# Performance work log

Measured on AMD Instinct MI355X. Metric: run time of the kernel, lower is better.

Reference implementation:

```python
import jax, jax.numpy as jnp
import numpy as np

B, N, HW, PS, FHW = 16, 4096, 224, 8, 56

def _gelu(x):
    return jax.nn.gelu(x, approximate=True)  # tanh approximation, matches nn.GELU(approximate='tanh')

def _conv(x, w, b, stride):
    y = jax.lax.conv_general_dilated(x, w, (stride, stride), [(1, 1), (1, 1)],
                                     dimension_numbers=('NCHW', 'OIHW', 'NCHW'))
    return y + b[None, :, None, None]

def _embed(points):
    # for i in 0..11: append sin(2^i * p) then cos(2^i * p) -> [B,N,48]
    factors = 2.0 ** jnp.arange(12, dtype=points.dtype)
    scaled = points[..., None, :] * factors[:, None]          # [B,N,12,2]
    feats = jnp.concatenate([jnp.sin(scaled), jnp.cos(scaled)], axis=-1)  # [B,N,12,4]
    return feats.reshape(points.shape[0], points.shape[1], 48)

def _extract_patches(fmap, points):
    # fmap [B,C,H,W]; points in [0,1]; bilinear grid_sample, zeros padding, align_corners=True
    Bq, C, H, W = fmap.shape
    centers = points * 2.0 - 1.0
    step = 2.0 / (W - 1)
    half = (PS - 1) / 2.0
    offs = jnp.linspace(-half, half, PS, dtype=fmap.dtype) * step
    offx2d, offy2d = jnp.meshgrid(offs, offs, indexing='ij')   # [ps,ps]
    gx = centers[..., 0][..., None, None] + offx2d             # [B,N,ps,ps]
    gy = centers[..., 1][..., None, None] + offy2d
    # align_corners=True pixel coords
    ix = (gx + 1.0) * 0.5 * (W - 1)
    iy = (gy + 1.0) * 0.5 * (H - 1)
    x0f = jnp.floor(ix); y0f = jnp.floor(iy)
    x0 = x0f.astype(jnp.int32); y0 = y0f.astype(jnp.int32)
    x1 = x0 + 1; y1 = y0 + 1
    wx1 = ix - x0f; wx0 = 1.0 - wx1
    wy1 = iy - y0f; wy0 = 1.0 - wy1
    fflat = fmap.reshape(Bq, C, H * W)

    def corner(xi, yi, w):
        valid = ((xi >= 0) & (xi < W) & (yi >= 0) & (yi < H)).astype(fmap.dtype)
        idx = jnp.clip(yi, 0, H - 1) * W + jnp.clip(xi, 0, W - 1)   # [B,N,ps,ps]
        vals = jax.vmap(lambda f, i: f[:, i])(fflat, idx)           # [B,C,N,ps,ps]
        return vals * (w * valid)[:, None]

    out = (corner(x0, y0, wx0 * wy0) + corner(x1, y0, wx1 * wy0)
           + corner(x0, y1, wx0 * wy1) + corner(x1, y1, wx1 * wy1))  # [B,C,N,ps,ps]
    return out.transpose(0, 2, 1, 3, 4)                              # [B,N,C,ps,ps]

def setup_inputs():
    key = jax.random.key(0)
    ks = jax.random.split(key, 26)
    def w(k, shape):
        fan_in = int(np.prod(shape[1:]))
        return jax.random.normal(k, shape, jnp.float32) * (1.0 / np.sqrt(fan_in))
    inp = {
        'points': jax.random.uniform(ks[0], (B, N, 2), jnp.float32),
        'images': jax.random.normal(ks[1], (B, 3, HW, HW), jnp.float32),
        # plane encoder
        'pw1': w(ks[2], (16, 3, 3, 3)),  'pb1': jnp.zeros((16,), jnp.float32),
        'pw2': w(ks[3], (32, 16, 3, 3)), 'pb2': jnp.zeros((32,), jnp.float32),
        'pw3': w(ks[4], (4, 32, 3, 3)),  'pb3': jnp.zeros((4,), jnp.float32),
        # global encoder
        'gw1': w(ks[5], (4, 3, 3, 3)),   'gb1': jnp.zeros((4,), jnp.float32),
        'gw2': w(ks[6], (8, 4, 3, 3)),   'gb2': jnp.zeros((8,), jnp.float32),
        'gw3': w(ks[7], (16, 8, 3, 3)),  'gb3': jnp.zeros((16,), jnp.float32),
        'gw4': w(ks[8], (32, 16, 3, 3)), 'gb4': jnp.zeros((32,), jnp.float32),
        'gw5': w(ks[9], (64, 32, 3, 3)), 'gb5': jnp.zeros((64,), jnp.float32),
        # point encoder (torch Linear: [out,in])
        'lw1': w(ks[10], (256, 48)),  'lb1': jnp.zeros((256,), jnp.float32),
        'lw2': w(ks[11], (256, 256)), 'lb2': jnp.zeros((256,), jnp.float32),
        # head
        'hw1': w(ks[12], (512, 576)), 'hb1': jnp.zeros((512,), jnp.float32),
        'hw2': w(ks[13], (1, 512)),   'hb2': jnp.zeros((1,), jnp.float32),
    }
    return inp

def reference(points, images, pw1, pb1, pw2, pb2, pw3, pb3,
              gw1, gb1, gw2, gb2, gw3, gb3, gw4, gb4, gw5, gb5,
              lw1, lb1, lw2, lb2, hw1, hb1, hw2, hb2):
    # point branch
    pe = _embed(points)                                         # [B,N,48]
    pf = _gelu(pe @ lw1.T + lb1) @ lw2.T + lb2                  # [B,N,256]
    # plane encoder -> 4x56x56 fmap
    f = _gelu(_conv(images, pw1, pb1, 2))
    f = _gelu(_conv(f, pw2, pb2, 2))
    fmap = _gelu(_conv(f, pw3, pb3, 1))                         # [B,4,56,56]
    # global encoder -> [B,64]
    g = images
    for wg, bg in ((gw1, gb1), (gw2, gb2), (gw3, gb3), (gw4, gb4), (gw5, gb5)):
        g = _gelu(_conv(g, wg, bg, 2))
    gc = g.mean(axis=(2, 3))                                    # AvgPool2d(7)+Flatten -> [B,64]
    gc = jnp.broadcast_to(gc[:, None, :], (points.shape[0], points.shape[1], 64))
    # per-point bilinear patch gather
    patches = _extract_patches(fmap, points).reshape(points.shape[0], points.shape[1], -1)  # [B,N,256]
    fused = jnp.concatenate([pf, patches, gc], axis=-1)         # [B,N,576]
    logit = _gelu(fused @ hw1.T + hb1) @ hw2.T + hb2            # [B,N,1]
    return logit
```

## Files before the change

kernel.cpp:

```cpp
#include <hip/hip_runtime.h>
#include <math.h>

#define BB 16
#define NN 4096
#define M_TOT (BB*NN)
#define HBK 64

typedef __attribute__((ext_vector_type(8))) short s8v;
typedef __attribute__((ext_vector_type(4))) float f4v;

__device__ __forceinline__ float gelu_t(float x){
    float u = 1.5957691216057308f * x * (1.0f + 0.044715f*x*x);
    return x / (1.0f + __expf(-u));
}

__device__ __forceinline__ unsigned short f2bf(float f){
    unsigned int u = __float_as_uint(f);
    u += 0x7fffu + ((u >> 16) & 1u);
    return (unsigned short)(u >> 16);
}

#define GLL(src, dst) __builtin_amdgcn_global_load_lds( \
    (const __attribute__((address_space(1))) void*)(src), \
    (__attribute__((address_space(3))) void*)(dst), 16, 0, 0)

template<int CIN, int COUT, int STRIDE, int CHUNK>
__device__ __forceinline__ void conv_dev2(
    const float* __restrict__ in, const float* __restrict__ w,
    const float* __restrict__ bias, float* __restrict__ out,
    int Hin, int Win, int Hout, int Wout, int bx, int by, int b, float* tile)
{
    constexpr int IW = 15*STRIDE + 3;
    constexpr int IH = IW;
    constexpr int PITCH = IW + 1;
    int tid = threadIdx.x;
    int tx = tid & 15, ty = tid >> 4;
    int wo = bx*16 + tx;
    int ho = by*16 + ty;
    int win0 = bx*16*STRIDE - 1;
    int hin0 = by*16*STRIDE - 1;
    bool valid = (wo < Wout) && (ho < Hout);

    float acc[COUT];
    #pragma unroll
    for (int co = 0; co < COUT; ++co) acc[co] = bias[co];

    const float* ib = in + (size_t)(b*CIN)*Hin*Win;
    for (int ci0 = 0; ci0 < CIN; ci0 += CHUNK) {
        __syncthreads();
        for (int idx = tid; idx < CHUNK*IH*IW; idx += 256) {
            int c = idx / (IH*IW), rem = idx - c*(IH*IW);
            int r = rem / IW, cc = rem - r*IW;
            int hi = hin0 + r, wi = win0 + cc;
            float v = 0.f;
            if ((unsigned)hi < (unsigned)Hin && (unsigned)wi < (unsigned)Win)
                v = ib[(size_t)(ci0 + c)*Hin*Win + hi*Win + wi];
            tile[c*IH*PITCH + r*PITCH + cc] = v;
        }
        __syncthreads();
        for (int ci = 0; ci < CHUNK; ++ci) {
            float vv[9];
            const float* tb = tile + ci*IH*PITCH;
            #pragma unroll
            for (int kh = 0; kh < 3; ++kh)
                #pragma unroll
                for (int kw = 0; kw < 3; ++kw)
                    vv[kh*3+kw] = tb[(ty*STRIDE + kh)*PITCH + tx*STRIDE + kw];
            const float* wc = w + (ci0 + ci)*9;
            #pragma unroll
            for (int co = 0; co < COUT; ++co) {
                const float* wp = wc + co*CIN*9;
                #pragma unroll
                for (int k = 0; k < 9; ++k)
                    acc[co] = fmaf(vv[k], wp[k], acc[co]);
            }
        }
    }
    if (valid) {
        size_t obase = ((size_t)b*COUT)*Hout*Wout + (size_t)ho*Wout + wo;
        #pragma unroll
        for (int co = 0; co < COUT; ++co)
            out[obase + (size_t)co*Hout*Wout] = gelu_t(acc[co]);
    }
}

__global__ __launch_bounds__(256) void conv_dual_k(
    const float* __restrict__ in,
    const float* __restrict__ wA, const float* __restrict__ bA,
    const float* __restrict__ wB, const float* __restrict__ bB,
    float* __restrict__ outA, float* __restrict__ outB)
{
    __shared__ float tile[3*33*34];
    const int Hin = 224, Win = 224, Hout = 112, Wout = 112;
    int tid = threadIdx.x;
    int tx = tid & 15, ty = tid >> 4;
    int b = blockIdx.z;
    int wo = blockIdx.x*16 + tx;
    int ho = blockIdx.y*16 + ty;
    int win0 = blockIdx.x*32 - 1;
    int hin0 = blockIdx.y*32 - 1;

    const float* ib = in + (size_t)(b*3)*Hin*Win;
    for (int idx = tid; idx < 3*1089; idx += 256) {
        int c = idx / 1089, rem = idx - c*1089;
        int r = rem / 33, cc = rem - r*33;
        int hi = hin0 + r, wi = win0 + cc;
        float v = 0.f;
        if ((unsigned)hi < (unsigned)Hin && (unsigned)wi < (unsigned)Win)
            v = ib[(size_t)c*Hin*Win + hi*Win + wi];
        tile[c*33*34 + r*34 + cc] = v;
    }
    __syncthreads();

    float accA[16], accB[4];
    #pragma unroll
    for (int co = 0; co < 16; ++co) accA[co] = bA[co];
    #pragma unroll
    for (int co = 0; co < 4; ++co) accB[co] = bB[co];

    #pragma unroll
    for (int ci = 0; ci < 3; ++ci) {
        float vv[9];
        const float* tb = tile + ci*33*34;
        #pragma unroll
        for (int kh = 0; kh < 3; ++kh)
            #pragma unroll
            for (int kw = 0; kw < 3; ++kw)
                vv[kh*3+kw] = tb[(ty*2 + kh)*34 + tx*2 + kw];
        #pragma unroll
        for (int co = 0; co < 16; ++co) {
            const float* wp = wA + co*27 + ci*9;
            #pragma unroll
            for (int k = 0; k < 9; ++k) accA[co] = fmaf(vv[k], wp[k], accA[co]);
        }
        #pragma unroll
        for (int co = 0; co < 4; ++co) {
            const float* wp = wB + co*27 + ci*9;
            #pragma unroll
            for (int k = 0; k < 9; ++k) accB[co] = fmaf(vv[k], wp[k], accB[co]);
        }
    }
    size_t px = (size_t)ho*Wout + wo;
    #pragma unroll
    for (int co = 0; co < 16; ++co)
        outA[((size_t)(b*16 + co))*Hout*Wout + px] = gelu_t(accA[co]);
    #pragma unroll
    for (int co = 0; co < 4; ++co)
        outB[((size_t)(b*4 + co))*Hout*Wout + px] = gelu_t(accB[co]);
}

__global__ __launch_bounds__(256) void conv_pg2_k(
    const float* __restrict__ f1, const float* __restrict__ pw2, const float* __restrict__ pb2, float* __restrict__ f2,
    const float* __restrict__ g1, const float* __restrict__ gw2, const float* __restrict__ gb2, float* __restrict__ g2)
{
    __shared__ float tile[8*33*34];
    int z = blockIdx.z;
    if (z < 32) {
        int b = z >> 1, half = z & 1;
        conv_dev2<16,16,2,8>(f1 + (size_t)b*16*12544, pw2 + half*2304, pb2 + half*16,
                             f2 + ((size_t)(b*32 + half*16))*3136,
                             112,112, 56,56, blockIdx.x, blockIdx.y, 0, tile);
    } else {
        conv_dev2<4,8,2,4>(g1, gw2, gb2, g2, 112,112, 56,56, blockIdx.x, blockIdx.y, z-32, tile);
    }
}

__global__ __launch_bounds__(256) void conv_pg3_k(
    const float* __restrict__ f2, const float* __restrict__ pw3, const float* __restrict__ pb3, float4* __restrict__ fmap4,
    const float* __restrict__ g2, const float* __restrict__ gw3, const float* __restrict__ gb3, float* __restrict__ g3)
{
    __shared__ float tile[8*33*34];
    int z = blockIdx.z;
    if (z < 16) {
        int b = z;
        int idx = blockIdx.x*256 + threadIdx.x;
        if (idx >= 3136) return;
        int ho = idx / 56, wo = idx - ho*56;
        const float* ib = f2 + (size_t)b*32*3136;
        float acc[4];
        #pragma unroll
        for (int co = 0; co < 4; ++co) acc[co] = pb3[co];
        for (int ci = 0; ci < 32; ++ci) {
            const float* ic = ib + (size_t)ci*3136;
            #pragma unroll
            for (int kh = 0; kh < 3; ++kh) {
                int hi = ho - 1 + kh;
                if ((unsigned)hi >= 56u) continue;
                #pragma unroll
                for (int kw = 0; kw < 3; ++kw) {
                    int wi = wo - 1 + kw;
                    if ((unsigned)wi >= 56u) continue;
                    float v = ic[hi*56 + wi];
                    int wofs = ci*9 + kh*3 + kw;
                    #pragma unroll
                    for (int co = 0; co < 4; ++co)
                        acc[co] = fmaf(v, pw3[co*288 + wofs], acc[co]);
                }
            }
        }
        float4 o;
        o.x = gelu_t(acc[0]); o.y = gelu_t(acc[1]);
        o.z = gelu_t(acc[2]); o.w = gelu_t(acc[3]);
        fmap4[(size_t)b*3136 + idx] = o;
    } else {
        if (blockIdx.x >= 4) return;
        int bx = blockIdx.x & 1, by = blockIdx.x >> 1;
        conv_dev2<8,16,2,8>(g2, gw3, gb3, g3, 56,56, 28,28, bx, by, z-16, tile);
    }
}

__global__ __launch_bounds__(256) void k4_k(
    const float* __restrict__ g3, const float* __restrict__ w4,
    const float* __restrict__ b4, float* __restrict__ g4o,
    const float4* __restrict__ fmap4, const float* __restrict__ points,
    unsigned short* __restrict__ C)
{
    __shared__ float4 pt[4*81];
    int bid = blockIdx.x;
    int tid = threadIdx.x;
    if (bid < 392) {
        int idx = bid*256 + tid;
        int co = idx & 31;
        int t = idx >> 5;
        int b = t / 196, px = t - b*196;
        int ho = px / 14, wo = px - ho*14;
        const float* src = g3 + (size_t)b*16*784;
        const float* wp = w4 + co*144;
        float acc = b4[co];
        for (int ci = 0; ci < 16; ++ci) {
            #pragma unroll
            for (int kh = 0; kh < 3; ++kh) {
                int hi = ho*2 - 1 + kh;
                if ((unsigned)hi >= 28u) continue;
                #pragma unroll
                for (int kw = 0; kw < 3; ++kw) {
                    int wi = wo*2 - 1 + kw;
                    if ((unsigned)wi >= 28u) continue;
                    acc = fmaf(src[ci*784 + hi*28 + wi], wp[ci*9 + kh*3 + kw], acc);
                }
            }
        }
        g4o[(size_t)b*6272 + px*32 + co] = gelu_t(acc);
    } else {
        int task = (bid - 392)*256 + tid;
        int wv = tid >> 6, lane = tid & 63;
        size_t m = (size_t)(task >> 6);
        int ij = task & 63;
        int i = ij >> 3, j = ij & 7;
        int b = (int)(m >> 12);
        float px = points[m*2], py = points[m*2+1];
        float X = fmaf(px, 55.f, -3.5f);
        float Y = fmaf(py, 55.f, -3.5f);
        float xbf = floorf(X), ybf = floorf(Y);
        int xbase = (int)xbf, ybase = (int)ybf;
        float wx1 = X - xbf, wx0 = 1.f - wx1;
        float wy1 = Y - ybf, wy0 = 1.f - wy1;
        const float4* fb = fmap4 + (size_t)b*3136;
        float4* tp = pt + wv*81;

        {
            int r = lane / 9, c = lane - r*9;
            int y = ybase + r, x = xbase + c;
            float4 v = {0.f, 0.f, 0.f, 0.f};
            if ((unsigned)x < 56u && (unsigned)y < 56u) v = fb[y*56 + x];
            tp[lane] = v;
            int idx2 = 64 + lane;
            if (idx2 < 81) {
                int r2 = idx2 / 9, c2 = idx2 - r2*9;
                int y2 = ybase + r2, x2 = xbase + c2;
                float4 v2 = {0.f, 0.f, 0.f, 0.f};
                if ((unsigned)x2 < 56u && (unsigned)y2 < 56u) v2 = fb[y2*56 + x2];
                tp[idx2] = v2;
            }
        }
        __syncthreads();

        float4 f00 = tp[j*9 + i];
        float4 f10 = tp[j*9 + i + 1];
        float4 f01 = tp[j*9 + 9 + i];
        float4 f11 = tp[j*9 + 9 + i + 1];
        float4 v;
        v.x = wy0*(wx0*f00.x + wx1*f10.x) + wy1*(wx0*f01.x + wx1*f11.x);
        v.y = wy0*(wx0*f00.y + wx1*f10.y) + wy1*(wx0*f01.y + wx1*f11.y);
        v.z = wy0*(wx0*f00.z + wx1*f10.z) + wy1*(wx0*f01.z + wx1*f11.z);
        v.w = wy0*(wx0*f00.w + wx1*f10.w) + wy1*(wx0*f01.w + wx1*f11.w);
        ushort4 o;
        o.x = f2bf(v.x); o.y = f2bf(v.y); o.z = f2bf(v.z); o.w = f2bf(v.w);
        *(ushort4*)(C + m*512 + 256 + ij*4) = o;
    }
}

__global__ __launch_bounds__(256) void g5_k(
    const float* __restrict__ g4o, const float* __restrict__ w5,
    const float* __restrict__ b5, float* __restrict__ gc)
{
    int idx = blockIdx.x*256 + threadIdx.x;
    int co = idx & 63;
    int t = idx >> 6;
    int b = t / 49, px = t - b*49;
    int ho = px / 7, wo = px - ho*7;
    const float* src = g4o + (size_t)b*6272;
    const float* wp = w5 + co*288;
    float acc = b5[co];
    for (int ci = 0; ci < 32; ++ci) {
        #pragma unroll
        for (int kh = 0; kh < 3; ++kh) {
            int hi = ho*2 - 1 + kh;
            if ((unsigned)hi >= 14u) continue;
            #pragma unroll
            for (int kw = 0; kw < 3; ++kw) {
                int wi = wo*2 - 1 + kw;
                if ((unsigned)wi >= 14u) continue;
                acc = fmaf(src[(hi*14 + wi)*32 + ci], wp[ci*9 + kh*3 + kw], acc);
            }
        }
    }
    atomicAdd(&gc[b*64 + co], gelu_t(acc) * (1.0f/49.0f));
}

__global__ __launch_bounds__(256) void hgc_k(
    const float* __restrict__ gc, const float* __restrict__ hw1,
    const float* __restrict__ hb1, float* __restrict__ hgc)
{
    int idx = blockIdx.x*256 + threadIdx.x;
    int b = idx >> 9, n = idx & 511;
    const float* g = gc + b*64;
    const float* w = hw1 + (size_t)n*576 + 512;
    float s = hb1[n];
    #pragma unroll
    for (int c = 0; c < 64; ++c) s = fmaf(g[c], w[c], s);
    hgc[idx] = s;
}

__global__ void cvtall_k(const float* __restrict__ lw1, const float* __restrict__ lw2,
                         const float* __restrict__ hw1, unsigned short* __restrict__ blw1,
                         unsigned short* __restrict__ blw2, unsigned short* __restrict__ bhw1,
                         float* __restrict__ out, const float* __restrict__ b2,
                         float* __restrict__ gc){
    int i = blockIdx.x*blockDim.x + threadIdx.x;
    if (i < M_TOT) out[i] = b2[0];
    if (i < 1024) gc[i] = 0.f;
    if (i < 256*64) {
        int r = i >> 6, c = i & 63;
        blw1[i] = (c < 48) ? f2bf(lw1[r*48 + c]) : 0;
        return;
    }
    int j = i - 256*64;
    if (j < 256*256) { blw2[j] = f2bf(lw2[j]); return; }
    j -= 256*256;
    if (j < 512*576) {
        int n = j / 576, k = j - n*576;
        int src_k = k;
        if (k >= 256 && k < 512) {
            int s = k - 256;
            src_k = 256 + (s & 3)*64 + (s >> 2);
        }
        bhw1[j] = f2bf(hw1[(size_t)n*576 + src_k]);
    }
}

__global__ __launch_bounds__(512) void mlp12_k(
    const float* __restrict__ points,
    const unsigned short* __restrict__ W1, const float* __restrict__ b1,
    const unsigned short* __restrict__ W2, const float* __restrict__ b2,
    unsigned short* __restrict__ C)
{
    __shared__ unsigned short Pe[128*64];
    __shared__ unsigned short Hd[128*256];
    int tid = threadIdx.x;
    int wv = tid >> 6, lane = tid & 63;
    int q = lane >> 4, lr = lane & 15;
    int mi = wv >> 2, ni = wv & 3;
    size_t m0 = (size_t)blockIdx.x * 128;

    #pragma unroll
    for (int it = 0; it < 2; ++it) {
        int idx = it*512 + tid;
        int row = idx >> 3, seg = idx & 7;
        size_t m = m0 + row;
        float px = points[m*2], py = points[m*2+1];
        union { s8v v; unsigned short u[8]; } pk;
        #pragma unroll
        for (int j = 0; j < 8; ++j) {
            int k = seg*8 + j;
            unsigned short val = 0;
            if (k < 48) {
                int i2 = k >> 2, rr = k & 3;
                float f = (float)(1 << i2);
                float p = (rr & 1) ? py : px;
                float s = f * p;
                val = f2bf((rr < 2) ? __sinf(s) : __cosf(s));
            }
            pk.u[j] = val;
        }
        *(s8v*)(Pe + (row*8 + (seg ^ (row & 7)))*8) = pk.v;
    }
    __syncthreads();

    f4v acc1[4][4];
    #pragma unroll
    for (int i = 0; i < 4; ++i)
        #pragma unroll
        for (int j = 0; j < 4; ++j) acc1[i][j] = (f4v){0.f,0.f,0.f,0.f};

    #pragma unroll
    for (int kb = 0; kb < 2; ++kb) {
        int seg = kb*4 + q;
        s8v a[4], b[4];
        #pragma unroll
        for (int t = 0; t < 4; ++t) {
            int row = mi*64 + t*16 + lr;
            a[t] = *(const s8v*)(Pe + (row*8 + (seg ^ (row & 7)))*8);
        }
        #pragma unroll
        for (int t = 0; t < 4; ++t) {
            int n = ni*64 + t*16 + lr;
            b[t] = *(const s8v*)(W1 + n*64 + seg*8);
        }
        #pragma unroll
        for (int mt = 0; mt < 4; ++mt)
            #pragma unroll
            for (int nt = 0; nt < 4; ++nt)
                acc1[mt][nt] = __builtin_amdgcn_mfma_f32_16x16x32_bf16(a[mt], b[nt], acc1[mt][nt], 0, 0, 0);
    }
    {
        float b1v[4];
        #pragma unroll
        for (int nt = 0; nt < 4; ++nt) b1v[nt] = b1[ni*64 + nt*16 + lr];
        #pragma unroll
        for (int mt = 0; mt < 4; ++mt)
            #pragma unroll
            for (int r4 = 0; r4 < 4; ++r4) {
                int row = mi*64 + mt*16 + q*4 + r4;
                #pragma unroll
                for (int nt = 0; nt < 4; ++nt) {
                    int col = ni*64 + nt*16 + lr;
                    float v = gelu_t(acc1[mt][nt][r4] + b1v[nt]);
                    int p = (col >> 3) ^ (row & 7);
                    Hd[(row*32 + p)*8 + (col & 7)] = f2bf(v);
                }
            }
    }
    __syncthreads();

    f4v acc2[4][4];
    #pragma unroll
    for (int i = 0; i < 4; ++i)
        #pragma unroll
        for (int j = 0; j < 4; ++j) acc2[i][j] = (f4v){0.f,0.f,0.f,0.f};

    #pragma unroll 2
    for (int kt = 0; kt < 8; ++kt) {
        s8v a[4], b[4];
        #pragma unroll
        for (int t = 0; t < 4; ++t) {
            int n = ni*64 + t*16 + lr;
            b[t] = *(const s8v*)(W2 + (size_t)n*256 + kt*32 + q*8);
        }
        #pragma unroll
        for (int t = 0; t < 4; ++t) {
            int row = mi*64 + t*16 + lr;
            int p = (kt*4 + q) ^ (row & 7);
            a[t] = *(const s8v*)(Hd + (row*32 + p)*8);
        }
        #pragma unroll
        for (int mt = 0; mt < 4; ++mt)
            #pragma unroll
            for (int nt = 0; nt < 4; ++nt)
                acc2[mt][nt] = __builtin_amdgcn_mfma_f32_16x16x32_bf16(a[mt], b[nt], acc2[mt][nt], 0, 0, 0);
    }
    {
        float b2v[4];
        #pragma unroll
        for (int nt = 0; nt < 4; ++nt) b2v[nt] = b2[ni*64 + nt*16 + lr];
        #pragma unroll
        for (int mt = 0; mt < 4; ++mt)
            #pragma unroll
            for (int r4 = 0; r4 < 4; ++r4) {
                size_t m = m0 + mi*64 + mt*16 + q*4 + r4;
                #pragma unroll
                for (int nt = 0; nt < 4; ++nt) {
                    int n = ni*64 + nt*16 + lr;
                    C[m*512 + n] = f2bf(acc2[mt][nt][r4] + b2v[nt]);
                }
            }
    }
}

__global__ __launch_bounds__(256, 3) void gemm_hd_k(
    const unsigned short* __restrict__ A,
    const unsigned short* __restrict__ W,
    const float* __restrict__ hgc, const float* __restrict__ w2,
    float* __restrict__ out)
{
    __shared__ unsigned short As[64*HBK];
    __shared__ unsigned short Bs[256*HBK];
    __shared__ float red[4*64];
    int tid = threadIdx.x;
    int wv = tid >> 6, lane = tid & 63;
    int q = lane >> 4, lr = lane & 15;
    int nq = wv * 64;
    size_t m0 = (size_t)blockIdx.x * 64;
    int nbase = blockIdx.y * 256;
    int bimg = (int)(m0 >> 12);

    const unsigned short* srcA[2]; unsigned short* dstA[2];
    #pragma unroll
    for (int r = 0; r < 2; ++r) {
        int f = r*256 + tid;
        int row = f >> 3, sl = (f & 7) ^ (row & 7);
        srcA[r] = A + (m0 + row)*512 + sl*8;
        dstA[r] = As + f*8;
    }
    const unsigned short* srcB[8]; unsigned short* dstB[8];
    #pragma unroll
    for (int r = 0; r < 8; ++r) {
        int f = r*256 + tid;
        int row = f >> 3, sl = (f & 7) ^ (row & 7);
        srcB[r] = W + (size_t)(nbase + row)*576 + sl*8;
        dstB[r] = Bs + f*8;
    }

    f4v acc[4][4];
    #pragma unroll
    for (int i = 0; i < 4; ++i)
        #pragma unroll
        for (int j = 0; j < 4; ++j) acc[i][j] = (f4v){0.f,0.f,0.f,0.f};

    for (int k0 = 0; k0 < 512; k0 += HBK) {
        #pragma unroll
        for (int r = 0; r < 2; ++r) { GLL(srcA[r], dstA[r]); srcA[r] += HBK; }
        #pragma unroll
        for (int r = 0; r < 8; ++r) { GLL(srcB[r], dstB[r]); srcB[r] += HBK; }
        __syncthreads();
        #pragma unroll
        for (int kk = 0; kk < 2; ++kk) {
            s8v a[4], b[4];
            #pragma unroll
            for (int t = 0; t < 4; ++t) {
                int row = t*16 + lr;
                int ph = (kk*4 + q) ^ (row & 7);
                a[t] = *(const s8v*)(As + (row*8 + ph)*8);
            }
            #pragma unroll
            for (int t = 0; t < 4; ++t) {
                int row = nq + t*16 + lr;
                int ph = (kk*4 + q) ^ (row & 7);
                b[t] = *(const s8v*)(Bs + (row*8 + ph)*8);
            }
            #pragma unroll
            for (int mt = 0; mt < 4; ++mt)
                #pragma unroll
                for (int nt = 0; nt < 4; ++nt)
                    acc[mt][nt] = __builtin_amdgcn_mfma_f32_16x16x32_bf16(a[mt], b[nt], acc[mt][nt], 0, 0, 0);
        }
        __syncthreads();
    }
    float bv[4], w2v[4];
    #pragma unroll
    for (int nt = 0; nt < 4; ++nt) {
        int n = nbase + nq + nt*16 + lr;
        bv[nt] = hgc[bimg*512 + n];
        w2v[nt] = w2[n];
    }
    #pragma unroll
    for (int mt = 0; mt < 4; ++mt)
        #pragma unroll
        for (int r4 = 0; r4 < 4; ++r4) {
            int ml = mt*16 + q*4 + r4;
            float s = 0.f;
            #pragma unroll
            for (int nt = 0; nt < 4; ++nt)
                s += gelu_t(acc[mt][nt][r4] + bv[nt]) * w2v[nt];
            #pragma unroll
            for (int off = 8; off > 0; off >>= 1) s += __shfl_down(s, off, 16);
            if (lr == 0) red[wv*64 + ml] = s;
        }
    __syncthreads();
    if (tid < 64) {
        float t = red[tid] + red[64 + tid] + red[128 + tid] + red[192 + tid];
        atomicAdd(&out[m0 + tid], t);
    }
}

extern "C" void kernel_launch(void* const* d_in, const int* in_sizes, int n_in,
                              void* d_out, int out_size, void* d_ws, size_t ws_size,
                              hipStream_t stream) {
    const float* points = (const float*)d_in[0];
    const float* images = (const float*)d_in[1];
    const float* pw1 = (const float*)d_in[2];  const float* pb1 = (const float*)d_in[3];
    const float* pw2 = (const float*)d_in[4];  const float* pb2 = (const float*)d_in[5];
    const float* pw3 = (const float*)d_in[6];  const float* pb3 = (const float*)d_in[7];
    const float* gw1 = (const float*)d_in[8];  const float* gb1 = (const float*)d_in[9];
    const float* gw2 = (const float*)d_in[10]; const float* gb2 = (const float*)d_in[11];
    const float* gw3 = (const float*)d_in[12]; const float* gb3 = (const float*)d_in[13];
    const float* gw4 = (const float*)d_in[14]; const float* gb4 = (const float*)d_in[15];
    const float* gw5 = (const float*)d_in[16]; const float* gb5 = (const float*)d_in[17];
    const float* lw1 = (const float*)d_in[18]; const float* lb1 = (const float*)d_in[19];
    const float* lw2 = (const float*)d_in[20]; const float* lb2 = (const float*)d_in[21];
    const float* hw1 = (const float*)d_in[22]; const float* hb1 = (const float*)d_in[23];
    const float* hw2 = (const float*)d_in[24]; const float* hb2 = (const float*)d_in[25];
    float* out = (float*)d_out;

    char* base = (char*)d_ws;
    unsigned short* fused_b = (unsigned short*)base;
    float4* fmap4 = (float4*)(fused_b + (size_t)M_TOT*512);
    float* g3   = (float*)(fmap4 + (size_t)16*3136);
    float* g4o  = g3 + (size_t)16*16*784;
    float* gc   = g4o + (size_t)16*32*196;
    float* hgc  = gc + 1024;
    unsigned short* blw1 = (unsigned short*)(hgc + 16*512);
    unsigned short* blw2 = blw1 + 256*64;
    unsigned short* bhw1 = blw2 + 256*256;
    float* ct = (float*)base;
    float* f1 = ct;
    float* f2 = f1 + (size_t)16*16*112*112;
    float* g1 = f2 + (size_t)16*32*56*56;
    float* g2 = g1 + (size_t)16*4*112*112;

    cvtall_k<<<1472, 256, 0, stream>>>(lw1, lw2, hw1, blw1, blw2, bhw1, out, hb2, gc);
    conv_dual_k<<<dim3(7,7,16), 256, 0, stream>>>(images, pw1, pb1, gw1, gb1, f1, g1);
    conv_pg2_k<<<dim3(4,4,48), 256, 0, stream>>>(f1, pw2, pb2, f2, g1, gw2, gb2, g2);
    conv_pg3_k<<<dim3(13,1,32), 256, 0, stream>>>(f2, pw3, pb3, fmap4, g2, gw3, gb3, g3);
    k4_k<<<392 + 16384, 256, 0, stream>>>(g3, gw4, gb4, g4o, fmap4, points, fused_b);
    g5_k<<<196, 256, 0, stream>>>(g4o, gw5, gb5, gc);
    hgc_k<<<32, 256, 0, stream>>>(gc, hw1, hb1, hgc);
    mlp12_k<<<M_TOT/128, 512, 0, stream>>>(points, blw1, lb1, blw2, lb2, fused_b);
    gemm_hd_k<<<dim3(M_TOT/64, 2), 256, 0, stream>>>(fused_b, bhw1, hgc, hw2, out);
}
```

Baseline: 392.4 us.

## Double-buffer LDS tiles in head GEMM to overlap loads with MFMA

The head GEMM kernel now keeps two LDS buffers for the A and W tiles. It issues the global-to-LDS loads for the next K step before computing the current one, so there is one barrier per step instead of two. The reduction scratch array reuses the A buffer after a barrier. Doubling the LDS footprint lowers the occupancy target from 3 to 2 blocks per CU, which trades latency hiding from other waves for latency hiding within the block.

Result: slower. 403.7 us (+2.9%).

```diff
diff --git a/kernel.cpp b/kernel.cpp
--- a/kernel.cpp
+++ b/kernel.cpp
@@ -487,15 +487,14 @@
     }
 }
 
-__global__ __launch_bounds__(256, 3) void gemm_hd_k(
+__global__ __launch_bounds__(256, 2) void gemm_hd_k(
     const unsigned short* __restrict__ A,
     const unsigned short* __restrict__ W,
     const float* __restrict__ hgc, const float* __restrict__ w2,
     float* __restrict__ out)
 {
-    __shared__ unsigned short As[64*HBK];
-    __shared__ unsigned short Bs[256*HBK];
-    __shared__ float red[4*64];
+    __shared__ unsigned short As[2][64*HBK];
+    __shared__ unsigned short Bs[2][256*HBK];
     int tid = threadIdx.x;
     int wv = tid >> 6, lane = tid & 63;
     int q = lane >> 4, lr = lane & 15;
@@ -504,21 +503,21 @@
     int nbase = blockIdx.y * 256;
     int bimg = (int)(m0 >> 12);
 
-    const unsigned short* srcA[2]; unsigned short* dstA[2];
+    const unsigned short* srcA[2]; int dA[2];
     #pragma unroll
     for (int r = 0; r < 2; ++r) {
         int f = r*256 + tid;
         int row = f >> 3, sl = (f & 7) ^ (row & 7);
         srcA[r] = A + (m0 + row)*512 + sl*8;
-        dstA[r] = As + f*8;
-    }
-    const unsigned short* srcB[8]; unsigned short* dstB[8];
+        dA[r] = f*8;
+    }
+    const unsigned short* srcB[8]; int dB[8];
     #pragma unroll
     for (int r = 0; r < 8; ++r) {
         int f = r*256 + tid;
         int row = f >> 3, sl = (f & 7) ^ (row & 7);
         srcB[r] = W + (size_t)(nbase + row)*576 + sl*8;
-        dstB[r] = Bs + f*8;
+        dB[r] = f*8;
     }
 
     f4v acc[4][4];
@@ -527,12 +526,13 @@
         #pragma unroll
         for (int j = 0; j < 4; ++j) acc[i][j] = (f4v){0.f,0.f,0.f,0.f};
 
-    for (int k0 = 0; k0 < 512; k0 += HBK) {
-        #pragma unroll
-        for (int r = 0; r < 2; ++r) { GLL(srcA[r], dstA[r]); srcA[r] += HBK; }
-        #pragma unroll
-        for (int r = 0; r < 8; ++r) { GLL(srcB[r], dstB[r]); srcB[r] += HBK; }
-        __syncthreads();
+    auto STAGE = [&](int buf) {
+        #pragma unroll
+        for (int r = 0; r < 2; ++r) { GLL(srcA[r], &As[buf][dA[r]]); srcA[r] += HBK; }
+        #pragma unroll
+        for (int r = 0; r < 8; ++r) { GLL(srcB[r], &Bs[buf][dB[r]]); srcB[r] += HBK; }
+    };
+    auto COMPUTE = [&](int buf) {
         #pragma unroll
         for (int kk = 0; kk < 2; ++kk) {
             s8v a[4], b[4];
@@ -540,13 +540,13 @@
             for (int t = 0; t < 4; ++t) {
                 int row = t*16 + lr;
                 int ph = (kk*4 + q) ^ (row & 7);
-                a[t] = *(const s8v*)(As + (row*8 + ph)*8);
+                a[t] = *(const s8v*)(&As[buf][(row*8 + ph)*8]);
             }
             #pragma unroll
             for (int t = 0; t < 4; ++t) {
                 int row = nq + t*16 + lr;
                 int ph = (kk*4 + q) ^ (row & 7);
-                b[t] = *(const s8v*)(Bs + (row*8 + ph)*8);
+                b[t] = *(const s8v*)(&Bs[buf][(row*8 + ph)*8]);
             }
             #pragma unroll
             for (int mt = 0; mt < 4; ++mt)
@@ -554,8 +554,17 @@
                 for (int nt = 0; nt < 4; ++nt)
                     acc[mt][nt] = __builtin_amdgcn_mfma_f32_16x16x32_bf16(a[mt], b[nt], acc[mt][nt], 0, 0, 0);
         }
-        __syncthreads();
-    }
+    };
+
+    STAGE(0);
+    #pragma unroll 1
+    for (int t = 0; t < 3; ++t) {
+        __syncthreads(); STAGE(1); COMPUTE(0);
+        __syncthreads(); STAGE(0); COMPUTE(1);
+    }
+    __syncthreads(); STAGE(1); COMPUTE(0);
+    __syncthreads();            COMPUTE(1);
+
     float bv[4], w2v[4];
     #pragma unroll
     for (int nt = 0; nt < 4; ++nt) {
@@ -563,6 +572,8 @@
         bv[nt] = hgc[bimg*512 + n];
         w2v[nt] = w2[n];
     }
+    __syncthreads();
+    float* red = (float*)&As[0][0];
     #pragma unroll
     for (int mt = 0; mt < 4; ++mt)
         #pragma unroll
```

## Load head GEMM operands directly from global into registers, dropping LDS staging

Applied to the files above, without the earlier changes.

The head GEMM kernel no longer stages A and W tiles through shared memory with global_load_lds and barriers. Each lane now loads its MFMA fragments straight from global memory inside a fully unrolled K loop, and launch bounds are raised to 4 blocks per CU. This removes LDS traffic and __syncthreads, but gives up operand sharing across waves: every wave reads the same A rows again, and the 16-byte strided global loads depend on L1/L2 hits and add register pressure.

Result: slower. 464.3 us (+18.3%).

```diff
diff --git a/kernel.cpp b/kernel.cpp
--- a/kernel.cpp
+++ b/kernel.cpp
@@ -4,7 +4,6 @@
 #define BB 16
 #define NN 4096
 #define M_TOT (BB*NN)
-#define HBK 64
 
 typedef __attribute__((ext_vector_type(8))) short s8v;
 typedef __attribute__((ext_vector_type(4))) float f4v;
@@ -19,10 +18,6 @@
     u += 0x7fffu + ((u >> 16) & 1u);
     return (unsigned short)(u >> 16);
 }
-
-#define GLL(src, dst) __builtin_amdgcn_global_load_lds( \
-    (const __attribute__((address_space(1))) void*)(src), \
-    (__attribute__((address_space(3))) void*)(dst), 16, 0, 0)
 
 template<int CIN, int COUT, int STRIDE, int CHUNK>
 __device__ __forceinline__ void conv_dev2(
@@ -487,14 +482,12 @@
     }
 }
 
-__global__ __launch_bounds__(256, 3) void gemm_hd_k(
+__global__ __launch_bounds__(256, 4) void gemm_hd_k(
     const unsigned short* __restrict__ A,
     const unsigned short* __restrict__ W,
     const float* __restrict__ hgc, const float* __restrict__ w2,
     float* __restrict__ out)
 {
-    __shared__ unsigned short As[64*HBK];
-    __shared__ unsigned short Bs[256*HBK];
     __shared__ float red[4*64];
     int tid = threadIdx.x;
     int wv = tid >> 6, lane = tid & 63;
@@ -504,21 +497,12 @@
     int nbase = blockIdx.y * 256;
     int bimg = (int)(m0 >> 12);
 
-    const unsigned short* srcA[2]; unsigned short* dstA[2];
-    #pragma unroll
-    for (int r = 0; r < 2; ++r) {
-        int f = r*256 + tid;
-        int row = f >> 3, sl = (f & 7) ^ (row & 7);
-        srcA[r] = A + (m0 + row)*512 + sl*8;
-        dstA[r] = As + f*8;
-    }
-    const unsigned short* srcB[8]; unsigned short* dstB[8];
-    #pragma unroll
-    for (int r = 0; r < 8; ++r) {
-        int f = r*256 + tid;
-        int row = f >> 3, sl = (f & 7) ^ (row & 7);
-        srcB[r] = W + (size_t)(nbase + row)*576 + sl*8;
-        dstB[r] = Bs + f*8;
+    const unsigned short* aP[4];
+    const unsigned short* bP[4];
+    #pragma unroll
+    for (int t = 0; t < 4; ++t) {
+        aP[t] = A + (m0 + t*16 + lr)*512 + q*8;
+        bP[t] = W + (size_t)(nbase + nq + t*16 + lr)*576 + q*8;
     }
 
     f4v acc[4][4];
@@ -527,35 +511,20 @@
         #pragma unroll
         for (int j = 0; j < 4; ++j) acc[i][j] = (f4v){0.f,0.f,0.f,0.f};
 
-    for (int k0 = 0; k0 < 512; k0 += HBK) {
-        #pragma unroll
-        for (int r = 0; r < 2; ++r) { GLL(srcA[r], dstA[r]); srcA[r] += HBK; }
-        #pragma unroll
-        for (int r = 0; r < 8; ++r) { GLL(srcB[r], dstB[r]); srcB[r] += HBK; }
-        __syncthreads();
-        #pragma unroll
-        for (int kk = 0; kk < 2; ++kk) {
-            s8v a[4], b[4];
-            #pragma unroll
-            for (int t = 0; t < 4; ++t) {
-                int row = t*16 + lr;
-                int ph = (kk*4 + q) ^ (row & 7);
-                a[t] = *(const s8v*)(As + (row*8 + ph)*8);
-            }
-            #pragma unroll
-            for (int t = 0; t < 4; ++t) {
-                int row = nq + t*16 + lr;
-                int ph = (kk*4 + q) ^ (row & 7);
-                b[t] = *(const s8v*)(Bs + (row*8 + ph)*8);
-            }
-            #pragma unroll
-            for (int mt = 0; mt < 4; ++mt)
-                #pragma unroll
-                for (int nt = 0; nt < 4; ++nt)
-                    acc[mt][nt] = __builtin_amdgcn_mfma_f32_16x16x32_bf16(a[mt], b[nt], acc[mt][nt], 0, 0, 0);
-        }
-        __syncthreads();
-    }
+    #pragma unroll
+    for (int k0 = 0; k0 < 512; k0 += 32) {
+        s8v a[4], b[4];
+        #pragma unroll
+        for (int t = 0; t < 4; ++t) a[t] = *(const s8v*)(aP[t] + k0);
+        #pragma unroll
+        for (int t = 0; t < 4; ++t) b[t] = *(const s8v*)(bP[t] + k0);
+        #pragma unroll
+        for (int mt = 0; mt < 4; ++mt)
+            #pragma unroll
+            for (int nt = 0; nt < 4; ++nt)
+                acc[mt][nt] = __builtin_amdgcn_mfma_f32_16x16x32_bf16(a[mt], b[nt], acc[mt][nt], 0, 0, 0);
+    }
+
     float bv[4], w2v[4];
     #pragma unroll
     for (int nt = 0; nt < 4; ++nt) {
```
